# Kernel optimization log

Measured on AMD Instinct MI355X. Metric: run time of the kernel, lower is better.

## Reference

```python
import jax, jax.numpy as jnp
import numpy as np

NUM_ITEMS, NUM_USERS, H = 100000, 16384, 48
GCN, ATTN, HID, TOW = 128, 128, 256, 256


def setup_inputs() -> dict:
    key = jax.random.key(0)
    ks = jax.random.split(key, 20)
    s = 0.02
    return {
        'item_feat': jax.random.normal(ks[0], (NUM_ITEMS, 2), jnp.float32),
        'gcn_item_emb': jax.random.normal(ks[1], (NUM_ITEMS, GCN), jnp.float32),
        'gcn_user_emb': jax.random.normal(ks[2], (NUM_USERS, GCN), jnp.float32),
        'hist_idx': jax.random.randint(ks[3], (NUM_USERS, H), 0, NUM_ITEMS, jnp.int32),
        'hist_len': jax.random.randint(ks[4], (NUM_USERS,), 0, H, jnp.int32),
        'Wi1': s * jax.random.normal(ks[5], (GCN + 2, HID), jnp.float32),
        'bi1': jnp.zeros((HID,), jnp.float32),
        'Wi2': s * jax.random.normal(ks[6], (HID, TOW), jnp.float32),
        'bi2': jnp.zeros((TOW,), jnp.float32),
        'Wq': s * jax.random.normal(ks[7], (GCN, ATTN), jnp.float32),
        'bq': jnp.zeros((ATTN,), jnp.float32),
        'Wk': s * jax.random.normal(ks[8], (TOW, ATTN), jnp.float32),
        'bk': jnp.zeros((ATTN,), jnp.float32),
        'Wu1': s * jax.random.normal(ks[9], (GCN + TOW, HID), jnp.float32),
        'bu1': jnp.zeros((HID,), jnp.float32),
        'Wu2': s * jax.random.normal(ks[10], (HID, TOW), jnp.float32),
        'bu2': jnp.zeros((TOW,), jnp.float32),
    }


def _l2norm(x):
    # F.normalize(dim=1): divide by L2 norm clamped to 1e-12
    n = jnp.sqrt(jnp.sum(x * x, axis=1, keepdims=True))
    return x / jnp.maximum(n, 1e-12)


def reference(item_feat, gcn_item_emb, gcn_user_emb, hist_idx, hist_len,
              Wi1, bi1, Wi2, bi2, Wq, bq, Wk, bk, Wu1, bu1, Wu2, bu2):
    # encode_items: [N, 130] -> MLP -> normalized [N, TOW]
    xi = jnp.concatenate([item_feat, gcn_item_emb], axis=1)
    h = jax.nn.relu(xi @ Wi1 + bi1)
    item_emb = _l2norm(h @ Wi2 + bi2)

    # encode_users (batched ragged attention with padding mask)
    item_vecs = item_emb[hist_idx]                       # [U, H, TOW]
    q = gcn_user_emb @ Wq + bq                           # [U, ATTN]
    k = item_vecs @ Wk + bk                              # [U, H, ATTN]
    scores = jnp.einsum('ud,uhd->uh', q, k) / jnp.sqrt(jnp.float32(ATTN))
    mask = jnp.arange(H)[None, :] <= hist_len[:, None]   # >= 1 valid per user
    attn = jax.nn.softmax(jnp.where(mask, scores, -1e30), axis=1)
    hist = jnp.einsum('uh,uhd->ud', attn, item_vecs)     # [U, TOW]
    fused = jnp.concatenate([gcn_user_emb, hist], axis=1)  # [U, 384]
    hu = jax.nn.relu(fused @ Wu1 + bu1)
    user_emb = _l2norm(hu @ Wu2 + bu2)
    return user_emb
```

## Files before the change

### kernel.cpp

```cpp
#include <hip/hip_runtime.h>
#include <hip/hip_bf16.h>
#include <hip/hip_fp8.h>
#include <math.h>

#define NITEMS 100000
#define NUSERS 16384
#define HLEN   48
#define GCN    128
#define ATTN_D 128
#define HID    256
#define TOW    256

typedef __attribute__((ext_vector_type(8))) short short8;
typedef __attribute__((ext_vector_type(16))) unsigned char uchar16;
typedef __attribute__((ext_vector_type(4))) float f32x4;
typedef __hip_bfloat16 bf16;

static __device__ __forceinline__ float bfu(unsigned short u) {
  unsigned int x = ((unsigned int)u) << 16;
  float f; __builtin_memcpy(&f, &x, 4); return f;
}
static __device__ __forceinline__ short f2bf(float v) {
  bf16 h = __float2bfloat16(v);
  short s; __builtin_memcpy(&s, &h, 2); return s;
}
static __device__ __forceinline__ unsigned char f2e4m3(float v) {
  __hip_fp8_e4m3 t(v);
  return (unsigned char)t.__x;
}
static __device__ __forceinline__ float e4m3f(unsigned char b) {
  __hip_fp8_e4m3 t;
  t.__x = (__hip_fp8_storage_t)b;
  return (float)t;
}

#define GLDS16(g, l)                                                            \
  __builtin_amdgcn_global_load_lds(                                             \
      (const __attribute__((address_space(1))) unsigned int*)(g),               \
      (__attribute__((address_space(3))) unsigned int*)(l), 16, 0, 0)

__global__ __launch_bounds__(256) void k_prep_w(const float* __restrict__ W,
                                                bf16* __restrict__ out,
                                                int Korig, int KS, int NT, int perm) {
  int tid = blockIdx.x * 256 + threadIdx.x;
  int total = KS * NT * 512;
  if (tid >= total) return;
  int i  = tid & 7;
  int l  = (tid >> 3) & 63;
  int ct = (tid >> 9) % NT;
  int ks = (tid >> 9) / NT;
  int k   = ks * 32 + ((l >> 4) << 3) + i;
  int col = ct * 16 + (l & 15);
  int N = NT * 16;
  int srck = perm ? ((k < 128) ? (k + 2) : (k - 128)) : k;
  float v = (k < Korig) ? W[(size_t)srck * N + col] : 0.f;
  out[tid] = __float2bfloat16(v);
}

__global__ __launch_bounds__(256) void k_prep_w8(const float* __restrict__ W,
                                                 unsigned char* __restrict__ out,
                                                 int KS, int NT) {
  int tid = blockIdx.x * 256 + threadIdx.x;
  int total = KS * NT * 512;
  if (tid >= total) return;
  int i  = tid & 7;
  int l  = (tid >> 3) & 63;
  int ct = (tid >> 9) % NT;
  int ks = (tid >> 9) / NT;
  int k   = ks * 32 + ((l >> 4) << 3) + i;
  int col = ct * 16 + (l & 15);
  out[tid] = f2e4m3(W[(size_t)k * (NT * 16) + col]);
}

__global__ __launch_bounds__(256) void k_prep_user(const float* __restrict__ gcn_user,
                                                   bf16* __restrict__ fused) {
  int tid = blockIdx.x * 256 + threadIdx.x;
  if (tid >= NUSERS * GCN) return;
  int k = tid & 127;
  int u = tid >> 7;
  fused[(size_t)u * (GCN + TOW) + k] = __float2bfloat16(gcn_user[tid]);
}

__global__ __launch_bounds__(256) void k_fold(const float* __restrict__ Wq,
                                              const float* __restrict__ Wk,
                                              const float* __restrict__ bq,
                                              float* __restrict__ out) {
  const float INV_S = 0.08838834764831845f;
  const int t = threadIdx.x;
  const int b = blockIdx.x;
  if (b < 16) {
    __shared__ float wq[8][128];
    for (int s = t; s < 8 * 128; s += 256)
      wq[s >> 7][s & 127] = Wq[(size_t)(b * 8 + (s >> 7)) * ATTN_D + (s & 127)];
    __syncthreads();
    float acc[8] = {0.f, 0.f, 0.f, 0.f, 0.f, 0.f, 0.f, 0.f};
    for (int d = 0; d < 128; ++d) {
      const float wk = Wk[(size_t)t * ATTN_D + d];
      #pragma unroll
      for (int gg = 0; gg < 8; ++gg) acc[gg] = fmaf(wq[gg][d], wk, acc[gg]);
    }
    #pragma unroll
    for (int gg = 0; gg < 8; ++gg)
      out[(size_t)(b * 8 + gg) * TOW + t] = acc[gg] * INV_S;
  } else {
    float a = 0.f;
    for (int d = 0; d < 128; ++d)
      a = fmaf(bq[d], Wk[(size_t)t * ATTN_D + d], a);
    out[(size_t)128 * TOW + t] = a * INV_S;
  }
}

__global__ __launch_bounds__(512, 4) void k_item_g1(
    const float* __restrict__ feat,
    const float* __restrict__ gcn,
    const bf16* __restrict__ Wf,
    const float* __restrict__ Wi1raw,
    const float* __restrict__ bias,
    unsigned char* __restrict__ h_out,
    int ntiles)
{
  __shared__ bf16  bs[4 * 8192];
  __shared__ float wfeat[512];
  const int j = threadIdx.x;
  const int l = j & 63;
  const int w = j >> 6;
  const int r = l & 15, g = l >> 4;
  const int jb = (j & ~63) * 8;

  #pragma unroll
  for (int s = 0; s < 8; ++s)
    GLDS16(Wf + (size_t)s * 4096 + (size_t)j * 8, &bs[s * 4096 + jb]);
  wfeat[j] = Wi1raw[j];

  float bj[16];
  #pragma unroll
  for (int ct = 0; ct < 16; ++ct) bj[ct] = bias[ct * 16 + r];

  __syncthreads();

  for (int t = blockIdx.x; t < ntiles; t += gridDim.x) {
    const int R0 = t * 128 + w * 16;
    int arow = R0 + r; if (arow >= NITEMS) arow = NITEMS - 1;
    const float* grow = gcn + (size_t)arow * GCN;

    f32x4 acc[16];
    #pragma unroll
    for (int ct = 0; ct < 16; ++ct) acc[ct] = (f32x4){0.f, 0.f, 0.f, 0.f};

    #pragma unroll 1
    for (int ks = 0; ks < 4; ++ks) {
      const float4* p = (const float4*)(grow + ks * 32 + g * 8);
      float4 x = p[0], y = p[1];
      short8 a;
      a[0] = f2bf(x.x); a[1] = f2bf(x.y); a[2] = f2bf(x.z); a[3] = f2bf(x.w);
      a[4] = f2bf(y.x); a[5] = f2bf(y.y); a[6] = f2bf(y.z); a[7] = f2bf(y.w);
      const bf16* wb = bs + (size_t)(ks * 16) * 512 + (size_t)l * 8;
      #pragma unroll
      for (int ct = 0; ct < 16; ++ct) {
        short8 b = *(const short8*)(wb + ct * 512);
        acc[ct] = __builtin_amdgcn_mfma_f32_16x16x32_bf16(a, b, acc[ct], 0, 0, 0);
      }
    }

    float f0[4], f1[4];
    #pragma unroll
    for (int i = 0; i < 4; ++i) {
      int orow = R0 + g * 4 + i; if (orow >= NITEMS) orow = NITEMS - 1;
      float2 fv = *(const float2*)(feat + (size_t)orow * 2);
      f0[i] = fv.x; f1[i] = fv.y;
    }
    #pragma unroll
    for (int ct = 0; ct < 16; ++ct) {
      const float w0 = wfeat[ct * 16 + r];
      const float w1 = wfeat[256 + ct * 16 + r];
      #pragma unroll
      for (int i = 0; i < 4; ++i) {
        float v = acc[ct][i] + bj[ct];
        v = fmaf(f0[i], w0, v);
        v = fmaf(f1[i], w1, v);
        h_out[(size_t)(R0 + g * 4 + i) * 256 + ct * 16 + r] =
            f2e4m3(fmaxf(v, 0.f));
      }
    }
  }
}

__global__ __launch_bounds__(512, 4) void k_gemm2_f8(
    const unsigned char* __restrict__ A8,
    const unsigned char* __restrict__ Wf8,
    const float* __restrict__ bias,
    unsigned char* __restrict__ Cout,
    int ntiles)
{
  __shared__ unsigned char bs8[8 * 8192];
  const int j = threadIdx.x;
  const int l = j & 63;
  const int w = j >> 6;
  const int r = l & 15, g = l >> 4;
  const int jb = (j & ~63) * 16;

  #pragma unroll
  for (int s = 0; s < 8; ++s)
    GLDS16(Wf8 + (size_t)s * 8192 + (size_t)j * 16, &bs8[s * 8192 + jb]);

  __syncthreads();

  for (int t = blockIdx.x; t < ntiles; t += gridDim.x) {
    const int R0 = t * 128 + w * 16;
    const unsigned char* arow = A8 + (size_t)(R0 + r) * 256 + g * 8;
    const unsigned char* wbase = bs8 + (size_t)l * 8;

    f32x4 acc[16];
    #pragma unroll
    for (int ct = 0; ct < 16; ++ct) acc[ct] = (f32x4){0.f, 0.f, 0.f, 0.f};

    #pragma unroll 1
    for (int ks = 0; ks < 8; ++ks) {
      long a;
      __builtin_memcpy(&a, arow + ks * 32, 8);
      const unsigned char* wb = wbase + (size_t)(ks * 16) * 512;
      #pragma unroll
      for (int ct = 0; ct < 16; ++ct) {
        long b;
        __builtin_memcpy(&b, wb + ct * 512, 8);
        acc[ct] = __builtin_amdgcn_mfma_f32_16x16x32_fp8_fp8(a, b, acc[ct], 0, 0, 0);
      }
    }

    float s[4] = {0.f, 0.f, 0.f, 0.f};
    #pragma unroll
    for (int ct = 0; ct < 16; ++ct) {
      const float bj = bias[ct * 16 + r];
      #pragma unroll
      for (int i = 0; i < 4; ++i) {
        acc[ct][i] += bj;
        s[i] += acc[ct][i] * acc[ct][i];
      }
    }
    #pragma unroll
    for (int off = 1; off < 16; off <<= 1) {
      #pragma unroll
      for (int i = 0; i < 4; ++i) s[i] += __shfl_xor(s[i], off);
    }
    float rn[4];
    #pragma unroll
    for (int i = 0; i < 4; ++i) rn[i] = 1.f / fmaxf(sqrtf(s[i]), 1e-12f);
    #pragma unroll
    for (int ct = 0; ct < 16; ++ct)
      #pragma unroll
      for (int i = 0; i < 4; ++i)
        Cout[(size_t)(R0 + g * 4 + i) * 256 + ct * 16 + r] =
            f2e4m3(acc[ct][i] * rn[i]);
  }
}

template<int KS, int NT, int MODE, int MR>
__global__ __launch_bounds__(256) void k_gemm(
    const bf16* __restrict__ A,
    const bf16* __restrict__ Wf,
    const float* __restrict__ bias,
    void* __restrict__ Cout,
    int Mtiles, int Astride)
{
  static_assert(NT % 4 == 0, "NT must be divisible by 4");
  constexpr int BSZ = NT * 512;
  constexpr int CH  = NT / 4;
  __shared__ bf16 bs[2][BSZ];
  const int j   = threadIdx.x;
  const int l   = j & 63;
  const int wid = j >> 6;
  int tile = blockIdx.x * 4 + wid;
  if (tile >= Mtiles) tile = Mtiles - 1;
  const int N = NT * 16;
  const int r = l & 15, g = l >> 4;

  {
    const short8* src = (const short8*)Wf;
    short8* dst = (short8*)bs[0];
    #pragma unroll
    for (int c = 0; c < CH; ++c) dst[c * 256 + j] = src[c * 256 + j];
  }

  f32x4 acc[MR][NT];
  #pragma unroll
  for (int mr = 0; mr < MR; ++mr)
    #pragma unroll
    for (int ct = 0; ct < NT; ++ct) acc[mr][ct] = (f32x4){0.f, 0.f, 0.f, 0.f};

  const bf16* arow[MR];
  #pragma unroll
  for (int mr = 0; mr < MR; ++mr)
    arow[mr] = A + (size_t)(tile * (16 * MR) + mr * 16 + r) * Astride + g * 8;

  __syncthreads();

  #pragma unroll
  for (int ks = 0; ks < KS; ++ks) {
    const int cur = ks & 1;
    short8 a[MR];
    #pragma unroll
    for (int mr = 0; mr < MR; ++mr) a[mr] = *(const short8*)(arow[mr] + ks * 32);
    short8 st[CH];
    if (ks + 1 < KS) {
      const short8* src = (const short8*)(Wf + (size_t)(ks + 1) * BSZ);
      #pragma unroll
      for (int c = 0; c < CH; ++c) st[c] = src[c * 256 + j];
    }
    const bf16* wb = bs[cur] + (size_t)l * 8;
    #pragma unroll
    for (int ct = 0; ct < NT; ++ct) {
      short8 b = *(const short8*)(wb + ct * 512);
      #pragma unroll
      for (int mr = 0; mr < MR; ++mr)
        acc[mr][ct] = __builtin_amdgcn_mfma_f32_16x16x32_bf16(a[mr], b, acc[mr][ct], 0, 0, 0);
    }
    if (ks + 1 < KS) {
      short8* dst = (short8*)bs[cur ^ 1];
      #pragma unroll
      for (int c = 0; c < CH; ++c) dst[c * 256 + j] = st[c];
    }
    __syncthreads();
  }

  #pragma unroll
  for (int mr = 0; mr < MR; ++mr) {
    #pragma unroll
    for (int ct = 0; ct < NT; ++ct) {
      const float bj = bias[ct * 16 + r];
      #pragma unroll
      for (int i = 0; i < 4; ++i) acc[mr][ct][i] += bj;
    }
  }

  if (MODE == 0 || MODE == 2 || MODE == 4) {
    #pragma unroll
    for (int mr = 0; mr < MR; ++mr)
      #pragma unroll
      for (int ct = 0; ct < NT; ++ct)
        #pragma unroll
        for (int i = 0; i < 4; ++i) {
          float v = acc[mr][ct][i];
          if (MODE == 0) v = fmaxf(v, 0.f);
          size_t off = (size_t)(tile * (16 * MR) + mr * 16 + g * 4 + i) * N + ct * 16 + r;
          if (MODE == 4) ((float*)Cout)[off] = v;
          else           ((bf16*)Cout)[off]  = __float2bfloat16(v);
        }
  } else {
    #pragma unroll
    for (int mr = 0; mr < MR; ++mr) {
      float s[4] = {0.f, 0.f, 0.f, 0.f};
      #pragma unroll
      for (int ct = 0; ct < NT; ++ct)
        #pragma unroll
        for (int i = 0; i < 4; ++i) s[i] += acc[mr][ct][i] * acc[mr][ct][i];
      #pragma unroll
      for (int off = 1; off < 16; off <<= 1) {
        #pragma unroll
        for (int i = 0; i < 4; ++i) s[i] += __shfl_xor(s[i], off);
      }
      float rn[4];
      #pragma unroll
      for (int i = 0; i < 4; ++i) rn[i] = 1.f / fmaxf(sqrtf(s[i]), 1e-12f);
      #pragma unroll
      for (int ct = 0; ct < NT; ++ct)
        #pragma unroll
        for (int i = 0; i < 4; ++i) {
          size_t off = (size_t)(tile * (16 * MR) + mr * 16 + g * 4 + i) * N + ct * 16 + r;
          float v = acc[mr][ct][i] * rn[i];
          if (MODE == 3) ((float*)Cout)[off] = v;
          else           ((bf16*)Cout)[off]  = __float2bfloat16(v);
        }
    }
  }
}

__global__ __launch_bounds__(256) void k_user_attn(
    const float* __restrict__ Qt,
    const int*   __restrict__ hist_idx,
    const int*   __restrict__ hist_len,
    const unsigned char* __restrict__ emb8,
    bf16* __restrict__ fused)
{
  const int wid = threadIdx.x >> 6, lane = threadIdx.x & 63;
  const int u = blockIdx.x * 4 + wid;
  const int g = lane >> 4, r = lane & 15;
  const int nv = hist_len[u] + 1;
  const int* uidx = hist_idx + (size_t)u * HLEN;

  const float* qp = Qt + (size_t)u * TOW + r * 16;
  f32x4 q0 = *(const f32x4*)(qp);
  f32x4 q1 = *(const f32x4*)(qp + 4);
  f32x4 q2 = *(const f32x4*)(qp + 8);
  f32x4 q3 = *(const f32x4*)(qp + 12);

  float l = 0.f;
  f32x4 O0 = (f32x4){0.f,0.f,0.f,0.f}, O1 = O0, O2 = O0, O3 = O0;

  int h = g;
  uchar16 e = (uchar16){0,0,0,0,0,0,0,0,0,0,0,0,0,0,0,0};
  if (h < nv)
    e = *(const uchar16*)(emb8 + (size_t)uidx[h] * TOW + r * 16);
  for (; h < nv; h += 4) {
    uchar16 en = (uchar16){0,0,0,0,0,0,0,0,0,0,0,0,0,0,0,0};
    if (h + 4 < nv)
      en = *(const uchar16*)(emb8 + (size_t)uidx[h + 4] * TOW + r * 16);
    float ef[16];
    #pragma unroll
    for (int i = 0; i < 16; ++i) ef[i] = e4m3f(e[i]);

    float sc = q0.x*ef[0] + q0.y*ef[1] + q0.z*ef[2] + q0.w*ef[3]
             + q1.x*ef[4] + q1.y*ef[5] + q1.z*ef[6] + q1.w*ef[7]
             + q2.x*ef[8] + q2.y*ef[9] + q2.z*ef[10]+ q2.w*ef[11]
             + q3.x*ef[12]+ q3.y*ef[13]+ q3.z*ef[14]+ q3.w*ef[15];
    #pragma unroll
    for (int off = 1; off < 16; off <<= 1) sc += __shfl_xor(sc, off);
    const float p = __expf(sc);
    l += p;
    O0.x += p*ef[0];  O0.y += p*ef[1];  O0.z += p*ef[2];  O0.w += p*ef[3];
    O1.x += p*ef[4];  O1.y += p*ef[5];  O1.z += p*ef[6];  O1.w += p*ef[7];
    O2.x += p*ef[8];  O2.y += p*ef[9];  O2.z += p*ef[10]; O2.w += p*ef[11];
    O3.x += p*ef[12]; O3.y += p*ef[13]; O3.z += p*ef[14]; O3.w += p*ef[15];
    e = en;
  }

  #pragma unroll
  for (int off = 16; off < 64; off <<= 1) {
    l += __shfl_xor(l, off);
    #pragma unroll
    for (int i = 0; i < 4; ++i) {
      O0[i] += __shfl_xor(O0[i], off);
      O1[i] += __shfl_xor(O1[i], off);
      O2[i] += __shfl_xor(O2[i], off);
      O3[i] += __shfl_xor(O3[i], off);
    }
  }

  if (g == 0) {
    const float inv = 1.f / l;
    short8 o0, o1;
    #pragma unroll
    for (int i = 0; i < 4; ++i) {
      o0[i]     = f2bf(O0[i] * inv);
      o0[4 + i] = f2bf(O1[i] * inv);
      o1[i]     = f2bf(O2[i] * inv);
      o1[4 + i] = f2bf(O3[i] * inv);
    }
    bf16* dst = fused + (size_t)u * (GCN + TOW) + GCN + r * 16;
    *(short8*)dst       = o0;
    *(short8*)(dst + 8) = o1;
  }
}

extern "C" void kernel_launch(void* const* d_in, const int* in_sizes, int n_in,
                              void* d_out, int out_size, void* d_ws, size_t ws_size,
                              hipStream_t stream) {
  const float* item_feat = (const float*)d_in[0];
  const float* gcn_item  = (const float*)d_in[1];
  const float* gcn_user  = (const float*)d_in[2];
  const int*   hist_idx  = (const int*)d_in[3];
  const int*   hist_len  = (const int*)d_in[4];
  const float* Wi1 = (const float*)d_in[5];
  const float* bi1 = (const float*)d_in[6];
  const float* Wi2 = (const float*)d_in[7];
  const float* bi2 = (const float*)d_in[8];
  const float* Wq  = (const float*)d_in[9];
  const float* bq  = (const float*)d_in[10];
  const float* Wk  = (const float*)d_in[11];
  const float* bk  = (const float*)d_in[12];
  const float* Wu1 = (const float*)d_in[13];
  const float* bu1 = (const float*)d_in[14];
  const float* Wu2 = (const float*)d_in[15];
  const float* bu2 = (const float*)d_in[16];
  (void)bk;

  char* ws = (char*)d_ws;
  bf16*  Wi1p  = (bf16*)(ws + 0);
  unsigned char* Wi2p8 = (unsigned char*)(ws + 81920);
  bf16*  Wu1p  = (bf16*)(ws + 147456);
  bf16*  Wu2p  = (bf16*)(ws + 344064);
  float* Wqkf  = (float*)(ws + 475136);
  bf16*  Wqkp  = (bf16*)(ws + 607232);
  float* Qt    = (float*)(ws + 672768);
  unsigned char* h8   = (unsigned char*)(ws + 17449984);
  unsigned char* emb8 = (unsigned char*)(ws + 43074560);
  bf16*  fusedA   = (bf16*)(ws + 68699136);
  bf16*  hu_buf   = (bf16*)(ws + 81282048);

  k_prep_w<<<160, 256, 0, stream>>>(Wi1, Wi1p, 130, 5, 16, 1);
  k_prep_w8<<<256, 256, 0, stream>>>(Wi2, Wi2p8, 8, 16);
  k_prep_w<<<384, 256, 0, stream>>>(Wu1, Wu1p, 384, 12, 16, 0);
  k_prep_w<<<256, 256, 0, stream>>>(Wu2, Wu2p, 256, 8, 16, 0);
  k_fold<<<17, 256, 0, stream>>>(Wq, Wk, bq, Wqkf);
  k_prep_w<<<128, 256, 0, stream>>>(Wqkf, Wqkp, 128, 4, 16, 0);
  k_prep_user<<<8192, 256, 0, stream>>>(gcn_user, fusedA);

  const int i128 = (NITEMS + 127) / 128;
  k_item_g1<<<512, 512, 0, stream>>>(item_feat, gcn_item, Wi1p, Wi1, bi1, h8, i128);
  k_gemm2_f8<<<512, 512, 0, stream>>>(h8, Wi2p8, bi2, emb8, i128);

  const int utiles = NUSERS / 32;
  const int ublk = utiles / 4;
  k_gemm<4, 16, 4, 2><<<ublk, 256, 0, stream>>>(fusedA, Wqkp, Wqkf + 128 * 256, Qt, utiles, 384);
  k_user_attn<<<NUSERS / 4, 256, 0, stream>>>(Qt, hist_idx, hist_len, emb8, fusedA);
  k_gemm<12, 16, 0, 2><<<ublk, 256, 0, stream>>>(fusedA, Wu1p, bu1, hu_buf, utiles, 384);
  k_gemm<8, 16, 3, 2><<<ublk, 256, 0, stream>>>(hu_buf, Wu2p, bu2, (float*)d_out, utiles, 256);
}
```

Before: 142.0 us.

## Merge weight-prep kernels into one launch and deepen attention gather prefetch

Seven small preprocessing kernels (weight packing, fp8 conversion, Wq·Wk fold, user-embedding copy) are merged into a single kernel whose block index selects the task. The Wq·Wk fold is now computed directly in packed bf16 layout, which removes the intermediate fp32 buffer and one dependent launch. The user-attention loop now prefetches two history rows ahead instead of one, to hide gather latency. This reduces launch overhead and serialization, at the cost of a less efficient per-element fold (each output does its own 128-length dot product) and extra registers in the attention kernel.

Result: faster. 121.9 us (-14.1%).

```diff
diff --git a/kernel.cpp b/kernel.cpp
--- a/kernel.cpp
+++ b/kernel.cpp
@@ -39,12 +39,9 @@
       (const __attribute__((address_space(1))) unsigned int*)(g),               \
       (__attribute__((address_space(3))) unsigned int*)(l), 16, 0, 0)
 
-__global__ __launch_bounds__(256) void k_prep_w(const float* __restrict__ W,
-                                                bf16* __restrict__ out,
-                                                int Korig, int KS, int NT, int perm) {
-  int tid = blockIdx.x * 256 + threadIdx.x;
-  int total = KS * NT * 512;
-  if (tid >= total) return;
+static __device__ __forceinline__ void packw_bf16(
+    const float* __restrict__ W, bf16* __restrict__ out,
+    int tid, int Korig, int NT, int perm) {
   int i  = tid & 7;
   int l  = (tid >> 3) & 63;
   int ct = (tid >> 9) % NT;
@@ -57,56 +54,57 @@
   out[tid] = __float2bfloat16(v);
 }
 
-__global__ __launch_bounds__(256) void k_prep_w8(const float* __restrict__ W,
-                                                 unsigned char* __restrict__ out,
-                                                 int KS, int NT) {
-  int tid = blockIdx.x * 256 + threadIdx.x;
-  int total = KS * NT * 512;
-  if (tid >= total) return;
-  int i  = tid & 7;
-  int l  = (tid >> 3) & 63;
-  int ct = (tid >> 9) % NT;
-  int ks = (tid >> 9) / NT;
-  int k   = ks * 32 + ((l >> 4) << 3) + i;
-  int col = ct * 16 + (l & 15);
-  out[tid] = f2e4m3(W[(size_t)k * (NT * 16) + col]);
-}
-
-__global__ __launch_bounds__(256) void k_prep_user(const float* __restrict__ gcn_user,
-                                                   bf16* __restrict__ fused) {
-  int tid = blockIdx.x * 256 + threadIdx.x;
-  if (tid >= NUSERS * GCN) return;
-  int k = tid & 127;
-  int u = tid >> 7;
-  fused[(size_t)u * (GCN + TOW) + k] = __float2bfloat16(gcn_user[tid]);
-}
-
-__global__ __launch_bounds__(256) void k_fold(const float* __restrict__ Wq,
-                                              const float* __restrict__ Wk,
-                                              const float* __restrict__ bq,
-                                              float* __restrict__ out) {
+__global__ __launch_bounds__(256) void k_prep_all(
+    const float* __restrict__ Wi1, const float* __restrict__ Wi2,
+    const float* __restrict__ Wu1, const float* __restrict__ Wu2,
+    const float* __restrict__ Wq,  const float* __restrict__ Wk,
+    const float* __restrict__ bq,  const float* __restrict__ gcn_user,
+    bf16* __restrict__ Wi1p, unsigned char* __restrict__ Wi2p8,
+    bf16* __restrict__ Wu1p, bf16* __restrict__ Wu2p,
+    bf16* __restrict__ Wqkp, float* __restrict__ bqt,
+    bf16* __restrict__ fused)
+{
   const float INV_S = 0.08838834764831845f;
+  const int b = blockIdx.x;
   const int t = threadIdx.x;
-  const int b = blockIdx.x;
-  if (b < 16) {
-    __shared__ float wq[8][128];
-    for (int s = t; s < 8 * 128; s += 256)
-      wq[s >> 7][s & 127] = Wq[(size_t)(b * 8 + (s >> 7)) * ATTN_D + (s & 127)];
-    __syncthreads();
-    float acc[8] = {0.f, 0.f, 0.f, 0.f, 0.f, 0.f, 0.f, 0.f};
-    for (int d = 0; d < 128; ++d) {
-      const float wk = Wk[(size_t)t * ATTN_D + d];
-      #pragma unroll
-      for (int gg = 0; gg < 8; ++gg) acc[gg] = fmaf(wq[gg][d], wk, acc[gg]);
-    }
-    #pragma unroll
-    for (int gg = 0; gg < 8; ++gg)
-      out[(size_t)(b * 8 + gg) * TOW + t] = acc[gg] * INV_S;
+  if (b < 160) {
+    packw_bf16(Wi1, Wi1p, b * 256 + t, 130, 16, 1);
+  } else if (b < 416) {
+    int tid = (b - 160) * 256 + t;
+    int i  = tid & 7;
+    int l  = (tid >> 3) & 63;
+    int ct = (tid >> 9) % 16;
+    int ks = (tid >> 9) / 16;
+    int k   = ks * 32 + ((l >> 4) << 3) + i;
+    int col = ct * 16 + (l & 15);
+    Wi2p8[tid] = f2e4m3(Wi2[(size_t)k * 256 + col]);
+  } else if (b < 800) {
+    packw_bf16(Wu1, Wu1p, (b - 416) * 256 + t, 384, 16, 0);
+  } else if (b < 1056) {
+    packw_bf16(Wu2, Wu2p, (b - 800) * 256 + t, 256, 16, 0);
+  } else if (b < 1184) {
+    int tid = (b - 1056) * 256 + t;
+    int i  = tid & 7;
+    int l  = (tid >> 3) & 63;
+    int ct = (tid >> 9) % 16;
+    int ks = (tid >> 9) / 16;
+    int k   = ks * 32 + ((l >> 4) << 3) + i;
+    int col = ct * 16 + (l & 15);
+    float a = 0.f;
+    const float* wq = Wq + (size_t)k * ATTN_D;
+    const float* wk = Wk + (size_t)col * ATTN_D;
+    for (int d = 0; d < 128; ++d) a = fmaf(wq[d], wk[d], a);
+    Wqkp[tid] = __float2bfloat16(a * INV_S);
+  } else if (b == 1184) {
+    float a = 0.f;
+    const float* wk = Wk + (size_t)t * ATTN_D;
+    for (int d = 0; d < 128; ++d) a = fmaf(bq[d], wk[d], a);
+    bqt[t] = a * INV_S;
   } else {
-    float a = 0.f;
-    for (int d = 0; d < 128; ++d)
-      a = fmaf(bq[d], Wk[(size_t)t * ATTN_D + d], a);
-    out[(size_t)128 * TOW + t] = a * INV_S;
+    int tid = (b - 1185) * 256 + t;
+    int k = tid & 127;
+    int u = tid >> 7;
+    fused[(size_t)u * (GCN + TOW) + k] = __float2bfloat16(gcn_user[tid]);
   }
 }
 
@@ -396,14 +394,18 @@
   float l = 0.f;
   f32x4 O0 = (f32x4){0.f,0.f,0.f,0.f}, O1 = O0, O2 = O0, O3 = O0;
 
-  int h = g;
-  uchar16 e = (uchar16){0,0,0,0,0,0,0,0,0,0,0,0,0,0,0,0};
-  if (h < nv)
-    e = *(const uchar16*)(emb8 + (size_t)uidx[h] * TOW + r * 16);
-  for (; h < nv; h += 4) {
-    uchar16 en = (uchar16){0,0,0,0,0,0,0,0,0,0,0,0,0,0,0,0};
-    if (h + 4 < nv)
-      en = *(const uchar16*)(emb8 + (size_t)uidx[h + 4] * TOW + r * 16);
+  uchar16 cur = (uchar16){0,0,0,0,0,0,0,0,0,0,0,0,0,0,0,0};
+  uchar16 nxt = cur;
+  if (g < nv)
+    cur = *(const uchar16*)(emb8 + (size_t)uidx[g] * TOW + r * 16);
+  if (g + 4 < nv)
+    nxt = *(const uchar16*)(emb8 + (size_t)uidx[g + 4] * TOW + r * 16);
+
+  for (int h = g; h < nv; h += 4) {
+    const uchar16 e = cur;
+    cur = nxt;
+    if (h + 8 < nv)
+      nxt = *(const uchar16*)(emb8 + (size_t)uidx[h + 8] * TOW + r * 16);
     float ef[16];
     #pragma unroll
     for (int i = 0; i < 16; ++i) ef[i] = e4m3f(e[i]);
@@ -420,7 +422,6 @@
     O1.x += p*ef[4];  O1.y += p*ef[5];  O1.z += p*ef[6];  O1.w += p*ef[7];
     O2.x += p*ef[8];  O2.y += p*ef[9];  O2.z += p*ef[10]; O2.w += p*ef[11];
     O3.x += p*ef[12]; O3.y += p*ef[13]; O3.z += p*ef[14]; O3.w += p*ef[15];
-    e = en;
   }
 
   #pragma unroll
@@ -478,21 +479,16 @@
   unsigned char* Wi2p8 = (unsigned char*)(ws + 81920);
   bf16*  Wu1p  = (bf16*)(ws + 147456);
   bf16*  Wu2p  = (bf16*)(ws + 344064);
-  float* Wqkf  = (float*)(ws + 475136);
-  bf16*  Wqkp  = (bf16*)(ws + 607232);
-  float* Qt    = (float*)(ws + 672768);
-  unsigned char* h8   = (unsigned char*)(ws + 17449984);
-  unsigned char* emb8 = (unsigned char*)(ws + 43074560);
-  bf16*  fusedA   = (bf16*)(ws + 68699136);
-  bf16*  hu_buf   = (bf16*)(ws + 81282048);
-
-  k_prep_w<<<160, 256, 0, stream>>>(Wi1, Wi1p, 130, 5, 16, 1);
-  k_prep_w8<<<256, 256, 0, stream>>>(Wi2, Wi2p8, 8, 16);
-  k_prep_w<<<384, 256, 0, stream>>>(Wu1, Wu1p, 384, 12, 16, 0);
-  k_prep_w<<<256, 256, 0, stream>>>(Wu2, Wu2p, 256, 8, 16, 0);
-  k_fold<<<17, 256, 0, stream>>>(Wq, Wk, bq, Wqkf);
-  k_prep_w<<<128, 256, 0, stream>>>(Wqkf, Wqkp, 128, 4, 16, 0);
-  k_prep_user<<<8192, 256, 0, stream>>>(gcn_user, fusedA);
+  bf16*  Wqkp  = (bf16*)(ws + 475136);
+  float* bqt   = (float*)(ws + 540672);
+  float* Qt    = (float*)(ws + 541696);
+  unsigned char* h8   = (unsigned char*)(ws + 17318912);
+  unsigned char* emb8 = (unsigned char*)(ws + 42943488);
+  bf16*  fusedA   = (bf16*)(ws + 68568064);
+  bf16*  hu_buf   = (bf16*)(ws + 81150976);
+
+  k_prep_all<<<9377, 256, 0, stream>>>(Wi1, Wi2, Wu1, Wu2, Wq, Wk, bq, gcn_user,
+                                       Wi1p, Wi2p8, Wu1p, Wu2p, Wqkp, bqt, fusedA);
 
   const int i128 = (NITEMS + 127) / 128;
   k_item_g1<<<512, 512, 0, stream>>>(item_feat, gcn_item, Wi1p, Wi1, bi1, h8, i128);
@@ -500,7 +496,7 @@
 
   const int utiles = NUSERS / 32;
   const int ublk = utiles / 4;
-  k_gemm<4, 16, 4, 2><<<ublk, 256, 0, stream>>>(fusedA, Wqkp, Wqkf + 128 * 256, Qt, utiles, 384);
+  k_gemm<4, 16, 4, 2><<<ublk, 256, 0, stream>>>(fusedA, Wqkp, bqt, Qt, utiles, 384);
   k_user_attn<<<NUSERS / 4, 256, 0, stream>>>(Qt, hist_idx, hist_len, emb8, fusedA);
   k_gemm<12, 16, 0, 2><<<ublk, 256, 0, stream>>>(fusedA, Wu1p, bu1, hu_buf, utiles, 384);
   k_gemm<8, 16, 3, 2><<<ublk, 256, 0, stream>>>(hu_buf, Wu2p, bu2, (float*)d_out, utiles, 256);
```
